# Optimization experiments

Measured on AMD Instinct MI355X. Metric: run time of the kernel, lower is better.

## Reference

```python
import jax, jax.numpy as jnp
import numpy as np

B, L, S = 8192, 1024, 3
OUTSIDE, TM_HELIX, INSIDE = 0, 1, 2


def setup_inputs() -> dict:
    key = jax.random.key(0)
    k1, k2 = jax.random.split(key)
    emissions = jax.random.normal(k1, (B, L, S), dtype=jnp.float32)
    tags = jax.random.randint(k2, (B, L), 0, S)
    mask = jnp.ones((B, L), dtype=jnp.float32)
    t = np.zeros((S, S), dtype=np.float32)
    t[OUTSIDE, INSIDE] = -5.0
    t[INSIDE, OUTSIDE] = -5.0
    t[OUTSIDE, TM_HELIX] = 1.0
    t[INSIDE, TM_HELIX] = 1.0
    t[TM_HELIX, OUTSIDE] = 1.0
    t[TM_HELIX, INSIDE] = 1.0
    transitions = jnp.asarray(t)
    return {"emissions": emissions, "mask": mask, "transitions": transitions, "tags": tags}


def _score_sentence(emissions, tags, mask, transitions):
    # emission score of the gold tag at every position: (B, L)
    em_score = jnp.take_along_axis(emissions, tags[..., None], axis=2)[..., 0]
    # transition score between consecutive gold tags: (B, L-1)
    trans_score = transitions[tags[:, :-1], tags[:, 1:]]
    return em_score[:, 0] * mask[:, 0] + jnp.sum(
        (trans_score + em_score[:, 1:]) * mask[:, 1:], axis=1
    )


def _forward_alg(emissions, mask, transitions):
    def step(alpha, xs):
        em_t, m_t = xs  # (B, S), (B,)
        # scores[b, i, j] = alpha[b, i] + T[i, j] + em_t[b, j]
        scores = alpha[:, :, None] + transitions[None, :, :] + em_t[:, None, :]
        new_alpha = jax.nn.logsumexp(scores, axis=1)
        alpha = jnp.where(m_t[:, None] > 0, new_alpha, alpha)
        return alpha, None

    alpha0 = emissions[:, 0, :]
    xs = (jnp.swapaxes(emissions[:, 1:, :], 0, 1),  # (L-1, B, S)
          jnp.swapaxes(mask[:, 1:], 0, 1))          # (L-1, B)
    alpha, _ = jax.lax.scan(step, alpha0, xs)
    return jax.nn.logsumexp(alpha, axis=1)  # (B,)


def reference(emissions, mask, transitions, tags):
    logZ = _forward_alg(emissions, mask, transitions)
    gold = _score_sentence(emissions, tags, mask, transitions)
    return jnp.mean(logZ - gold)
```

## Files before the change

### kernel.cpp

```cpp
#include <hip/hip_runtime.h>


#define LOG2E 1.4426950408889634f
#define LN2   0.6931471805599453f

constexpr int B = 8192;
constexpr int L = 1024;
constexpr int SEQS_PER_BLOCK = 4;

__device__ __forceinline__ float fexp2(float x) { return __builtin_amdgcn_exp2f(x); }
__device__ __forceinline__ float flog2(float x) { return __builtin_amdgcn_logf(x); }

__device__ __forceinline__ float f4get(const float4& v, int c) {
  return c == 0 ? v.x : (c == 1 ? v.y : (c == 2 ? v.z : v.w));
}

__device__ __forceinline__ float mux3(float x0, float x1, float x2, int i) {
  return (i == 0) ? x0 : ((i == 1) ? x1 : x2);
}

__device__ __forceinline__ void renorm3(float* __restrict__ P, float& scale) {
  float m = P[0];
  #pragma unroll
  for (int e = 1; e < 9; ++e) m = fmaxf(m, P[e]);
  int ex;
  (void)frexpf(m, &ex);
  #pragma unroll
  for (int e = 0; e < 9; ++e) P[e] = ldexpf(P[e], -ex);
  scale += (float)ex;
}

__global__ __launch_bounds__(256, 4) void crf_main(
    const float* __restrict__ em, const float* __restrict__ mask,
    const float* __restrict__ trans, const int* __restrict__ tags,
    float* __restrict__ out) {
  const int lane = threadIdx.x & 63;
  const int wid = threadIdx.x >> 6;
  const int b = blockIdx.x * SEQS_PER_BLOCK + wid;

  __shared__ float sT2[12];
  __shared__ float red[SEQS_PER_BLOCK];
  if (threadIdx.x < 9) sT2[threadIdx.x] = trans[threadIdx.x] * LOG2E;
  __syncthreads();

  const float4* emp = (const float4*)(em + (size_t)b * (L * 3)) + lane * 12;
  const float4* mkp = (const float4*)(mask + (size_t)b * L) + lane * 4;
  const int4*   tgp = (const int4*)(tags + (size_t)b * L) + lane * 4;

  float tk[9];
  #pragma unroll
  for (int e = 0; e < 9; ++e) tk[e] = fexp2(trans[e] * LOG2E);

  float P[9] = {1.f, 0.f, 0.f, 0.f, 1.f, 0.f, 0.f, 0.f, 1.f};
  float scale = 0.f, gold = 0.f;
  float a0 = 0.f, a1 = 0.f, a2 = 0.f;
  float e0_sel = 0.f, mk0 = 0.f;
  int tag0 = 0, prev = 0;

  #pragma unroll 1
  for (int g = 0; g < 4; ++g) {
    const float4 E0 = emp[3 * g + 0];
    const float4 E1 = emp[3 * g + 1];
    const float4 E2 = emp[3 * g + 2];
    const float4 MKg = mkp[g];
    const int4 tg = tgp[g];
    const int tp = tg.x | (tg.y << 2) | (tg.z << 4) | (tg.w << 6);

    #pragma unroll
    for (int q = 0; q < 4; ++q) {
      const int i0 = 3 * q + 0, i1 = 3 * q + 1, i2 = 3 * q + 2;
      const float ev0 = f4get(i0 < 4 ? E0 : (i0 < 8 ? E1 : E2), i0 & 3) * LOG2E;
      const float ev1 = f4get(i1 < 4 ? E0 : (i1 < 8 ? E1 : E2), i1 & 3) * LOG2E;
      const float ev2 = f4get(i2 < 4 ? E0 : (i2 < 8 ? E1 : E2), i2 & 3) * LOG2E;
      const float m   = f4get(MKg, q);
      const int   cur = (tp >> (2 * q)) & 3;

      const float e = mux3(ev0, ev1, ev2, cur);
      if (q == 0 && g == 0) {
        e0_sel = e; mk0 = m; tag0 = cur;
      } else {
        gold = fmaf(sT2[3 * prev + cur] + e, m, gold);
      }
      prev = cur;

      const float w0 = fexp2(ev0);
      const float w1 = fexp2(ev1);
      const float w2 = fexp2(ev2);
      if (q == 0 && g == 0) { a0 = w0; a1 = w1; a2 = w2; }
      const bool first = (q == 0) && (g == 0);
      const bool act = (m > 0.f) && !(first && lane == 0);
      const float gg = act ? 1.f : 0.f;
      const float c1 = 1.f - gg;
      const float u0 = w0 * gg, u1 = w1 * gg, u2 = w2 * gg;
      float M[9];
      M[0] = fmaf(tk[0], u0, c1); M[1] = tk[1] * u1;           M[2] = tk[2] * u2;
      M[3] = tk[3] * u0;          M[4] = fmaf(tk[4], u1, c1);  M[5] = tk[5] * u2;
      M[6] = tk[6] * u0;          M[7] = tk[7] * u1;           M[8] = fmaf(tk[8], u2, c1);
      #pragma unroll
      for (int i = 0; i < 3; ++i) {
        const float p0 = P[3 * i + 0], p1 = P[3 * i + 1], p2 = P[3 * i + 2];
        P[3 * i + 0] = p0 * M[0] + p1 * M[3] + p2 * M[6];
        P[3 * i + 1] = p0 * M[1] + p1 * M[4] + p2 * M[7];
        P[3 * i + 2] = p0 * M[2] + p1 * M[5] + p2 * M[8];
      }
    }
    if (g & 1) renorm3(P, scale);
  }

  const int prevLast = __shfl_up(prev, 1);
  const float t0 = sT2[3 * prevLast + tag0];
  gold = fmaf((lane == 0 ? 0.f : t0) + e0_sel, mk0, gold);

  #pragma unroll 1
  for (int d = 1; d < 64; d <<= 1) {
    float o[9];
    #pragma unroll
    for (int e = 0; e < 9; ++e) o[e] = __shfl_xor(P[e], d, 64);
    const float osc = __shfl_xor(scale, d, 64);
    gold += __shfl_xor(gold, d, 64);
    const bool later = (lane & d) != 0;
    float A[9], Bm[9];
    #pragma unroll
    for (int e = 0; e < 9; ++e) {
      A[e]  = later ? o[e] : P[e];
      Bm[e] = later ? P[e] : o[e];
    }
    #pragma unroll
    for (int i = 0; i < 3; ++i) {
      const float p0 = A[3 * i + 0], p1 = A[3 * i + 1], p2 = A[3 * i + 2];
      P[3 * i + 0] = p0 * Bm[0] + p1 * Bm[3] + p2 * Bm[6];
      P[3 * i + 1] = p0 * Bm[1] + p1 * Bm[4] + p2 * Bm[7];
      P[3 * i + 2] = p0 * Bm[2] + p1 * Bm[5] + p2 * Bm[8];
    }
    scale += osc;
  }

  if (lane == 0) {
    const float z = a0 * (P[0] + P[1] + P[2]) +
                    a1 * (P[3] + P[4] + P[5]) +
                    a2 * (P[6] + P[7] + P[8]);
    red[wid] = LN2 * (scale + flog2(z) - gold);
  }
  __syncthreads();
  if (threadIdx.x == 0) {
    const float s = red[0] + red[1] + red[2] + red[3];
    atomicAdd(out, s * (1.0f / (float)B));
  }
}

extern "C" void kernel_launch(void* const* d_in, const int* in_sizes, int n_in,
                              void* d_out, int out_size, void* d_ws, size_t ws_size,
                              hipStream_t stream) {
  const float* em    = (const float*)d_in[0];
  const float* mask  = (const float*)d_in[1];
  const float* trans = (const float*)d_in[2];
  const int*   tags  = (const int*)d_in[3];
  float* out = (float*)d_out;

  hipMemsetAsync(out, 0, sizeof(float), stream);
  crf_main<<<B / SEQS_PER_BLOCK, 256, 0, stream>>>(em, mask, trans, tags, out);
}
```

Before: 220.4 us.

## Stage emissions into LDS via coalesced global_load_lds and pack mask/tags into bitfields

Emissions for each sequence are now copied with coalesced direct global-to-LDS loads, where consecutive lanes fetch consecutive float4s. Each lane then reads its own 12-float4 chunk from LDS instead of issuing strided per-lane global loads. Mask and tags are loaded up front and packed into bitfields to reduce register pressure and load latency inside the loop. The occupancy hint drops from 4 to 3 blocks per CU because of the 48KB LDS per block. This risks fewer waves in flight and LDS bank conflicts on the 12-float4-stride reads.

```diff
diff --git a/kernel.cpp b/kernel.cpp
--- a/kernel.cpp
+++ b/kernel.cpp
@@ -19,6 +19,14 @@
   return (i == 0) ? x0 : ((i == 1) ? x1 : x2);
 }
 
+__device__ __forceinline__ unsigned packmask4(const float4& v) {
+  return (unsigned)(v.x > 0.f) | ((unsigned)(v.y > 0.f) << 1) |
+         ((unsigned)(v.z > 0.f) << 2) | ((unsigned)(v.w > 0.f) << 3);
+}
+__device__ __forceinline__ unsigned packtag4(const int4& v) {
+  return (unsigned)(v.x | (v.y << 2) | (v.z << 4) | (v.w << 6));
+}
+
 __device__ __forceinline__ void renorm3(float* __restrict__ P, float& scale) {
   float m = P[0];
   #pragma unroll
@@ -30,7 +38,7 @@
   scale += (float)ex;
 }
 
-__global__ __launch_bounds__(256, 4) void crf_main(
+__global__ __launch_bounds__(256, 3) void crf_main(
     const float* __restrict__ em, const float* __restrict__ mask,
     const float* __restrict__ trans, const int* __restrict__ tags,
     float* __restrict__ out) {
@@ -38,18 +46,36 @@
   const int wid = threadIdx.x >> 6;
   const int b = blockIdx.x * SEQS_PER_BLOCK + wid;
 
+  __shared__ float4 sEm[SEQS_PER_BLOCK][768];
   __shared__ float sT2[12];
   __shared__ float red[SEQS_PER_BLOCK];
   if (threadIdx.x < 9) sT2[threadIdx.x] = trans[threadIdx.x] * LOG2E;
-  __syncthreads();
 
-  const float4* emp = (const float4*)(em + (size_t)b * (L * 3)) + lane * 12;
+  const float4* emG = (const float4*)em + (size_t)b * 768;
   const float4* mkp = (const float4*)(mask + (size_t)b * L) + lane * 4;
   const int4*   tgp = (const int4*)(tags + (size_t)b * L) + lane * 4;
+
+  const float4 M0 = mkp[0], M1 = mkp[1], M2 = mkp[2], M3 = mkp[3];
+  const int4   G0 = tgp[0], G1 = tgp[1], G2 = tgp[2], G3 = tgp[3];
+
+  #pragma unroll
+  for (int i = 0; i < 12; ++i) {
+    __builtin_amdgcn_global_load_lds(
+        (const __attribute__((address_space(1))) void*)(emG + 64 * i + lane),
+        (__attribute__((address_space(3))) void*)(&sEm[wid][64 * i]),
+        16, 0, 0);
+  }
+
+  const unsigned mpack = packmask4(M0) | (packmask4(M1) << 4) |
+                         (packmask4(M2) << 8) | (packmask4(M3) << 12);
+  const unsigned tpack = packtag4(G0) | (packtag4(G1) << 8) |
+                         (packtag4(G2) << 16) | (packtag4(G3) << 24);
 
   float tk[9];
   #pragma unroll
   for (int e = 0; e < 9; ++e) tk[e] = fexp2(trans[e] * LOG2E);
+
+  __syncthreads();
 
   float P[9] = {1.f, 0.f, 0.f, 0.f, 1.f, 0.f, 0.f, 0.f, 1.f};
   float scale = 0.f, gold = 0.f;
@@ -57,26 +83,25 @@
   float e0_sel = 0.f, mk0 = 0.f;
   int tag0 = 0, prev = 0;
 
+  const float4* myEm = &sEm[wid][lane * 12];
+
   #pragma unroll 1
-  for (int g = 0; g < 4; ++g) {
-    const float4 E0 = emp[3 * g + 0];
-    const float4 E1 = emp[3 * g + 1];
-    const float4 E2 = emp[3 * g + 2];
-    const float4 MKg = mkp[g];
-    const int4 tg = tgp[g];
-    const int tp = tg.x | (tg.y << 2) | (tg.z << 4) | (tg.w << 6);
+  for (int q = 0; q < 4; ++q) {
+    const float4 E0 = myEm[3 * q + 0];
+    const float4 E1 = myEm[3 * q + 1];
+    const float4 E2 = myEm[3 * q + 2];
 
     #pragma unroll
-    for (int q = 0; q < 4; ++q) {
-      const int i0 = 3 * q + 0, i1 = 3 * q + 1, i2 = 3 * q + 2;
+    for (int k = 0; k < 4; ++k) {
+      const int i0 = 3 * k + 0, i1 = 3 * k + 1, i2 = 3 * k + 2;
       const float ev0 = f4get(i0 < 4 ? E0 : (i0 < 8 ? E1 : E2), i0 & 3) * LOG2E;
       const float ev1 = f4get(i1 < 4 ? E0 : (i1 < 8 ? E1 : E2), i1 & 3) * LOG2E;
       const float ev2 = f4get(i2 < 4 ? E0 : (i2 < 8 ? E1 : E2), i2 & 3) * LOG2E;
-      const float m   = f4get(MKg, q);
-      const int   cur = (tp >> (2 * q)) & 3;
+      const float m   = ((mpack >> (4 * q + k)) & 1u) ? 1.f : 0.f;
+      const int   cur = (int)((tpack >> (8 * q + 2 * k)) & 3u);
 
       const float e = mux3(ev0, ev1, ev2, cur);
-      if (q == 0 && g == 0) {
+      if (k == 0 && q == 0) {
         e0_sel = e; mk0 = m; tag0 = cur;
       } else {
         gold = fmaf(sT2[3 * prev + cur] + e, m, gold);
@@ -86,8 +111,8 @@
       const float w0 = fexp2(ev0);
       const float w1 = fexp2(ev1);
       const float w2 = fexp2(ev2);
-      if (q == 0 && g == 0) { a0 = w0; a1 = w1; a2 = w2; }
-      const bool first = (q == 0) && (g == 0);
+      if (k == 0 && q == 0) { a0 = w0; a1 = w1; a2 = w2; }
+      const bool first = (k == 0) && (q == 0);
       const bool act = (m > 0.f) && !(first && lane == 0);
       const float gg = act ? 1.f : 0.f;
       const float c1 = 1.f - gg;
@@ -104,7 +129,7 @@
         P[3 * i + 2] = p0 * M[2] + p1 * M[5] + p2 * M[8];
       }
     }
-    if (g & 1) renorm3(P, scale);
+    if (q & 1) renorm3(P, scale);
   }
 
   const int prevLast = __shfl_up(prev, 1);
```

Measured after the change: 201.6 us. 1.09x faster.
